# Kernel tuning notes

Measured on AMD Instinct MI355X. Metric: run time of the kernel, lower is better.

Reference implementation:

```python
import jax, jax.numpy as jnp
import numpy as np

LN_EPS = 1e-5
NORM_EPS = 1e-12


def channel_layernorm(x, w, b):
    # LayerNorm over channel dim of NCHW tensor (torch permutes to NHWC; equivalent)
    mu = x.mean(axis=1, keepdims=True)
    var = x.var(axis=1, keepdims=True)
    xn = (x - mu) / jnp.sqrt(var + LN_EPS)
    return xn * w[None, :, None, None] + b[None, :, None, None]


def pconv(x, w):
    # 1x1 pointwise conv, w: (out_ch, in_ch)
    return jnp.einsum('bchw,oc->bohw', x, w)


def dwconv3(x, w):
    # depthwise 3x3, padding 1; w: (ch, 1, 3, 3)
    return jax.lax.conv_general_dilated(
        x, w, window_strides=(1, 1), padding='SAME',
        feature_group_count=x.shape[1],
        dimension_numbers=('NCHW', 'OIHW', 'NCHW'))


def l2norm(x):
    n = jnp.sqrt(jnp.sum(x * x, axis=-1, keepdims=True))
    return x / jnp.maximum(n, NORM_EPS)


def setup_inputs() -> dict:
    key = jax.random.key(0)
    ks = jax.random.split(key, 8)
    B, C, H, W = 4, 128, 128, 128
    NH, G = 8, 2

    def w(k, shape, fan_in):
        return jax.random.normal(k, shape, dtype=jnp.float32) * (fan_in ** -0.5)

    return {
        'x': jax.random.normal(ks[0], (B, C, H, W), dtype=jnp.float32),
        'ln1_w': jnp.ones((C,), jnp.float32),
        'ln1_b': jnp.zeros((C,), jnp.float32),
        'temperature': jnp.ones((NH, 1, 1), jnp.float32),
        'qkv_p_w': w(ks[1], (3 * C, C), C),
        'qkv_d_w': w(ks[2], (3 * C, 1, 3, 3), 9),
        'proj_w': w(ks[3], (C, C), C),
        'ln2_w': jnp.ones((C,), jnp.float32),
        'ln2_b': jnp.zeros((C,), jnp.float32),
        'g1_w': w(ks[4], (2 * G * C, C), C),
        'gd_w': w(ks[5], (2 * G * C, 1, 3, 3), 9),
        'g2_w': w(ks[6], (C, G * C), G * C),
        'num_heads': NH,
    }


def reference(x, ln1_w, ln1_b, temperature, qkv_p_w, qkv_d_w, proj_w,
              ln2_w, ln2_b, g1_w, gd_w, g2_w, num_heads):
    b, c, h, w_ = x.shape
    d = c // num_heads

    # --- MDTA branch ---
    y = channel_layernorm(x, ln1_w, ln1_b)
    qkv = dwconv3(pconv(y, qkv_p_w), qkv_d_w)  # (b, 3c, h, w)
    q, k, v = jnp.split(qkv, 3, axis=1)
    q = l2norm(q.reshape(b, num_heads, d, h * w_))
    k = l2norm(k.reshape(b, num_heads, d, h * w_))
    v = v.reshape(b, num_heads, d, h * w_)
    # transposed (channel) attention: (b, heads, d, d)
    attn = jnp.einsum('bhdn,bhen->bhde', q, k) * temperature[None]
    attn = jax.nn.softmax(attn, axis=-1)
    out = jnp.einsum('bhde,bhen->bhdn', attn, v).reshape(b, c, h, w_)
    x = x + pconv(out, proj_w)

    # --- GDFN branch ---
    y = channel_layernorm(x, ln2_w, ln2_b)
    hdn = dwconv3(pconv(y, g1_w), gd_w)  # (b, 2*gamma*c, h, w)
    x1, x2 = jnp.split(hdn, 2, axis=1)
    g = jax.nn.gelu(x1, approximate=False) * x2
    x = x + pconv(g, g2_w)
    return x
```

## Files before the change

kernel.cpp:

```cpp
#include <hip/hip_runtime.h>
#include <cstdint>
#include <cstddef>

typedef float f32x4 __attribute__((ext_vector_type(4)));
typedef __bf16 bf16x8 __attribute__((ext_vector_type(8)));

__device__ __forceinline__ float b2f(unsigned short u) {
    union { unsigned int i; float f; } z; z.i = ((unsigned int)u) << 16; return z.f;
}
__device__ __forceinline__ unsigned short f2b(float f) {
    union { float f; unsigned int i; } z; z.f = f;
    unsigned int x = z.i;
    return (unsigned short)((x + 0x7FFFu + ((x >> 16) & 1u)) >> 16);
}

static constexpr int C = 128;
static constexpr int NP = 16384;
static constexpr int NH = 8;

struct Ptr11 { const float* p[11]; };
__constant__ int kWN[11]   = {128, 128, 8, 49152, 3456, 16384, 128, 128, 65536, 4608, 32768};
__constant__ int kWOff[11] = {0, 128, 256, 272, 49424, 52880, 69264, 69392, 69520, 135056, 139664};
static constexpr int kWTotal = 172432;

__global__ __launch_bounds__(256)
void cvt_w_kernel(Ptr11 P, unsigned short* __restrict__ dst)
{
    int seg = blockIdx.y;
    int n = kWN[seg];
    int i = blockIdx.x * 256 + threadIdx.x;
    if (i >= n) return;
    dst[kWOff[seg] + i] = f2b(P.p[seg][i]);
}

__device__ __forceinline__ void dw8(const unsigned short* base, int y, int xi,
                                    const float* wr, float* o)
{
    uint4 rv0 = uint4{0,0,0,0}, rv1, rv2 = uint4{0,0,0,0};
    if (y > 0)   rv0 = *(const uint4*)(base - 128);
    rv1 = *(const uint4*)(base);
    if (y < 127) rv2 = *(const uint4*)(base + 128);
    uint4 rows[3] = {rv0, rv1, rv2};
    #pragma unroll
    for (int j = 0; j < 8; ++j) o[j] = 0.f;
    #pragma unroll
    for (int r = 0; r < 3; ++r) {
        union { uint4 v; unsigned short u[8]; } cv; cv.v = rows[r];
        int lh = __shfl_up((int)cv.u[7], 1, 16);
        int rh = __shfl_down((int)cv.u[0], 1, 16);
        float p[10];
        p[0] = (xi > 0)   ? b2f((unsigned short)lh) : 0.f;
        p[9] = (xi < 120) ? b2f((unsigned short)rh) : 0.f;
        #pragma unroll
        for (int j = 0; j < 8; ++j) p[j + 1] = b2f(cv.u[j]);
        #pragma unroll
        for (int j = 0; j < 8; ++j)
            o[j] += wr[r * 3] * p[j] + wr[r * 3 + 1] * p[j + 1] + wr[r * 3 + 2] * p[j + 2];
    }
}

template <int COUT>
__device__ __forceinline__ void gemm_core_tr(
    const unsigned short* BsT,
    const unsigned short* __restrict__ W,
    unsigned short* __restrict__ OutB,
    int n0, int tid)
{
    const int lane = tid & 63;
    const int wid  = tid >> 6;
    const int ln16 = lane & 15, quad = lane >> 4;
    const int wy = wid >> 1, wx = wid & 1;
    const char* bs = (const char*)BsT;
    const int swz = (ln16 & 7) << 4;
    int rbase[4];
    #pragma unroll
    for (int nt = 0; nt < 4; ++nt) {
        int n = wx * 64 + nt * 16 + ln16;
        rbase[nt] = n * 256 + quad * 16;
    }

    for (int cc = 0; cc < COUT / 128; ++cc) {
        const int m0 = cc * 128;
        f32x4 acc[4][4];
        #pragma unroll
        for (int i = 0; i < 4; ++i)
            #pragma unroll
            for (int j = 0; j < 4; ++j) acc[i][j] = f32x4{0.f, 0.f, 0.f, 0.f};

        #pragma unroll
        for (int k0 = 0; k0 < 128; k0 += 32) {
            bf16x8 afr[4], bfr[4];
            #pragma unroll
            for (int mt = 0; mt < 4; ++mt) {
                int m = m0 + wy * 64 + mt * 16 + ln16;
                uint4 v = *(const uint4*)(W + (size_t)m * 128 + k0 + quad * 8);
                afr[mt] = *(bf16x8*)&v;
            }
            #pragma unroll
            for (int nt = 0; nt < 4; ++nt) {
                uint4 v = *(const uint4*)(bs + ((rbase[nt] + k0 * 2) ^ swz));
                bfr[nt] = *(bf16x8*)&v;
            }
            #pragma unroll
            for (int mt = 0; mt < 4; ++mt)
                #pragma unroll
                for (int nt = 0; nt < 4; ++nt)
                    acc[mt][nt] = __builtin_amdgcn_mfma_f32_16x16x32_bf16(
                        afr[mt], bfr[nt], acc[mt][nt], 0, 0, 0);
        }
        #pragma unroll
        for (int mt = 0; mt < 4; ++mt)
            #pragma unroll
            for (int nt = 0; nt < 4; ++nt) {
                int co0 = m0 + wy * 64 + mt * 16 + quad * 4;
                int n = n0 + wx * 64 + nt * 16 + ln16;
                #pragma unroll
                for (int r = 0; r < 4; ++r)
                    OutB[(size_t)(co0 + r) * NP + n] = f2b(acc[mt][nt][r]);
            }
    }
}

template <int COUT>
__global__ __launch_bounds__(256)
void lngemm_kernel(const float* __restrict__ x,
                   const unsigned short* __restrict__ lg,
                   const unsigned short* __restrict__ lb,
                   const unsigned short* __restrict__ W,
                   unsigned short* __restrict__ Out)
{
    __shared__ unsigned short BsT[128 * 128];
    __shared__ float Ssum[8][128], Ssq[8][128], Mu[128], Rs[128];
    const int tid = threadIdx.x;
    const int b = blockIdx.y;
    const int n0 = blockIdx.x * 128;
    const int pxg = tid & 31;
    const int cseg = tid >> 5;
    const float* xb = x + (size_t)b * C * NP + n0 + pxg * 4;

    f32x4 hv[16];
    f32x4 vs = f32x4{0.f, 0.f, 0.f, 0.f}, vq = f32x4{0.f, 0.f, 0.f, 0.f};
    #pragma unroll
    for (int i = 0; i < 16; ++i) {
        f32x4 v = *(const f32x4*)(xb + (size_t)(cseg * 16 + i) * NP);
        hv[i] = v; vs += v; vq += v * v;
    }
    #pragma unroll
    for (int j = 0; j < 4; ++j) {
        Ssum[cseg][pxg * 4 + j] = vs[j];
        Ssq[cseg][pxg * 4 + j]  = vq[j];
    }
    __syncthreads();
    if (tid < 128) {
        float s = 0.f, q = 0.f;
        #pragma unroll
        for (int e = 0; e < 8; ++e) { s += Ssum[e][tid]; q += Ssq[e][tid]; }
        float mu = s * (1.f / 128.f);
        float var = q * (1.f / 128.f) - mu * mu;
        Mu[tid] = mu;
        Rs[tid] = rsqrtf(fmaxf(var, 0.f) + 1e-5f);
    }
    __syncthreads();
    f32x4 mu4 = *(const f32x4*)(&Mu[pxg * 4]);
    f32x4 rs4 = *(const f32x4*)(&Rs[pxg * 4]);

    float gwv[16], bwv[16];
    #pragma unroll
    for (int i = 0; i < 16; ++i) {
        gwv[i] = b2f(lg[cseg * 16 + i]);
        bwv[i] = b2f(lb[cseg * 16 + i]);
    }

    char* p = (char*)BsT;
    #pragma unroll
    for (int j = 0; j < 4; ++j) {
        int n = pxg * 4 + j;
        union { uint4 v[2]; unsigned short u[16]; } o;
        #pragma unroll
        for (int i = 0; i < 16; ++i)
            o.u[i] = f2b((hv[i][j] - mu4[j]) * rs4[j] * gwv[i] + bwv[i]);
        int base = n * 256 + cseg * 32;
        int sw = (n & 7) << 4;
        *(uint4*)(p + (base ^ sw))        = o.v[0];
        *(uint4*)(p + ((base + 16) ^ sw)) = o.v[1];
    }
    __syncthreads();
    gemm_core_tr<COUT>(BsT, W, Out + (size_t)b * COUT * NP, n0, tid);
}

template <int COUT>
__global__ __launch_bounds__(256)
void gemm_bf16t_kernel(const unsigned short* __restrict__ W,
                       const unsigned short* __restrict__ Xt,
                       unsigned short* __restrict__ Out)
{
    __shared__ unsigned short BsT[128 * 128];
    const int tid = threadIdx.x;
    const int b = blockIdx.y;
    const int n0 = blockIdx.x * 128;
    const unsigned short* Xb = Xt + (size_t)b * NP * 128 + (size_t)n0 * 128;
    char* p = (char*)BsT;
    #pragma unroll
    for (int r = 0; r < 8; ++r) {
        int flat = tid + r * 256;
        int n = flat >> 4, ks = flat & 15;
        uint4 v = *(const uint4*)(Xb + (size_t)n * 128 + ks * 8);
        *(uint4*)(p + ((n * 256 + ks * 16) ^ ((n & 7) << 4))) = v;
    }
    __syncthreads();
    gemm_core_tr<COUT>(BsT, W, Out + (size_t)b * COUT * NP, n0, tid);
}

__global__ __launch_bounds__(256)
void dwqkgram_kernel(const unsigned short* __restrict__ big,
                     const unsigned short* __restrict__ w9,
                     float* __restrict__ Spart,
                     float* __restrict__ Npart)
{
    __shared__ unsigned short qs_[16 * 520];
    __shared__ unsigned short ks_[16 * 520];
    __shared__ float Sred[4][256];
    const int h = blockIdx.x, b = blockIdx.y, sp = blockIdx.z;
    const int tid = threadIdx.x;
    const int wid = tid >> 6, lane = tid & 63;
    const int xi = (tid & 15) * 8;
    const int yr = (tid >> 4) & 3;
    const int y  = sp * 4 + yr;
    const int bh = b * NH + h;
    float* Np = Npart + ((size_t)bh * 32 + sp) * 32;

    #pragma unroll
    for (int p = 0; p < 4; ++p) {
        int qc = p * 4 + wid;
        #pragma unroll
        for (int s = 0; s < 2; ++s) {
            int ch = s * 128 + h * 16 + qc;
            const unsigned short* base = big + ((size_t)b * 384 + ch) * NP + y * 128 + xi;
            float wr[9];
            #pragma unroll
            for (int i = 0; i < 9; ++i) wr[i] = b2f(w9[ch * 9 + i]);
            float o[8];
            dw8(base, y, xi, wr, o);
            union { uint4 v; unsigned short u[8]; } res;
            float ss = 0.f;
            #pragma unroll
            for (int j = 0; j < 8; ++j) {
                res.u[j] = f2b(o[j]);
                float vv = b2f(res.u[j]);
                ss += vv * vv;
            }
            unsigned short* tile = s ? ks_ : qs_;
            *(uint4*)(&tile[qc * 520 + yr * 128 + xi]) = res.v;
            #pragma unroll
            for (int od = 32; od > 0; od >>= 1) ss += __shfl_xor(ss, od, 64);
            if (lane == 0) Np[s * 16 + qc] = ss;
        }
    }
    __syncthreads();

    const int ln16 = lane & 15, quad = lane >> 4;
    f32x4 acc = f32x4{0.f, 0.f, 0.f, 0.f};
    #pragma unroll
    for (int i = 0; i < 4; ++i) {
        int off = wid * 128 + i * 32 + quad * 8;
        uint4 qv = *(const uint4*)(&qs_[ln16 * 520 + off]);
        uint4 kv = *(const uint4*)(&ks_[ln16 * 520 + off]);
        acc = __builtin_amdgcn_mfma_f32_16x16x32_bf16(*(bf16x8*)&qv, *(bf16x8*)&kv, acc, 0, 0, 0);
    }
    #pragma unroll
    for (int r = 0; r < 4; ++r) Sred[wid][(quad * 4 + r) * 16 + ln16] = acc[r];
    __syncthreads();
    float ssum = Sred[0][tid] + Sred[1][tid] + Sred[2][tid] + Sred[3][tid];
    Spart[((size_t)bh * 32 + sp) * 256 + tid] = ssum;
}

__global__ __launch_bounds__(256)
void softwp_kernel(const float* __restrict__ Spart, const float* __restrict__ Npart,
                   const unsigned short* __restrict__ temp,
                   const unsigned short* __restrict__ proj,
                   unsigned short* __restrict__ W2)
{
    __shared__ float Ps[256];
    int bh = blockIdx.x;
    int b = bh >> 3, h = bh & 7;
    int t = threadIdx.x;
    int dq = t >> 4, dk = t & 15;
    float sacc = 0.f;
    const float* Sp = Spart + (size_t)bh * 32 * 256;
    #pragma unroll
    for (int j = 0; j < 32; ++j) sacc += Sp[j * 256 + t];
    const float* Np = Npart + (size_t)bh * 32 * 32;
    float sq = 0.f, sk = 0.f;
    #pragma unroll
    for (int sp = 0; sp < 32; ++sp) { sq += Np[sp * 32 + dq]; sk += Np[sp * 32 + 16 + dk]; }
    float nq = fmaxf(sqrtf(sq), 1e-12f);
    float nk = fmaxf(sqrtf(sk), 1e-12f);
    float v = sacc / (nq * nk) * b2f(temp[h]);
    float m = v;
    #pragma unroll
    for (int o = 8; o > 0; o >>= 1) m = fmaxf(m, __shfl_xor(m, o, 16));
    float e = __expf(v - m);
    float s = e;
    #pragma unroll
    for (int o = 8; o > 0; o >>= 1) s += __shfl_xor(s, o, 16);
    Ps[t] = e / s;
    __syncthreads();

    int co = t >> 1;
    int eo = (t & 1) * 8;
    union { uint4 v[2]; unsigned short u[16]; } pw;
    pw.v[0] = *(const uint4*)(proj + (size_t)co * 128 + h * 16);
    pw.v[1] = *(const uint4*)(proj + (size_t)co * 128 + h * 16 + 8);
    float prw[16];
    #pragma unroll
    for (int d = 0; d < 16; ++d) prw[d] = b2f(pw.u[d]);
    union { uint4 v; unsigned short u[8]; } o8;
    #pragma unroll
    for (int j = 0; j < 8; ++j) {
        int ee = eo + j;
        float s2 = 0.f;
        #pragma unroll
        for (int d = 0; d < 16; ++d) s2 += prw[d] * Ps[d * 16 + ee];
        o8.u[j] = f2b(s2);
    }
    *(uint4*)(W2 + ((size_t)b * 128 + co) * 128 + h * 16 + eo) = o8.v;
}

__global__ __launch_bounds__(256)
void projln_kernel(const unsigned short* __restrict__ W2,
                   const unsigned short* __restrict__ big,
                   const unsigned short* __restrict__ w9,
                   const float* __restrict__ Res,
                   unsigned short* __restrict__ Xmid,
                   const unsigned short* __restrict__ lg,
                   const unsigned short* __restrict__ lb,
                   unsigned short* __restrict__ Y2t)
{
    __shared__ unsigned short Bs[128][130];
    __shared__ float RedS[2][128], RedQ[2][128], Mu[128], Rs[128];
    const int tid = threadIdx.x;
    const int b = blockIdx.y;
    const int y = blockIdx.x;
    const int n0 = y * 128;
    const unsigned short* Wb = W2 + (size_t)b * 16384;

    {
        const int xi = (tid & 15) * 8;
        const int crow = tid >> 4;
        #pragma unroll
        for (int p = 0; p < 8; ++p) {
            int c = p * 16 + crow;
            int ch = 256 + c;
            const unsigned short* base = big + ((size_t)b * 384 + ch) * NP + n0 + xi;
            float wr[9];
            #pragma unroll
            for (int i = 0; i < 9; ++i) wr[i] = b2f(w9[ch * 9 + i]);
            float o[8];
            dw8(base, y, xi, wr, o);
            union { uint4 v; unsigned int d[4]; unsigned short u[8]; } res;
            #pragma unroll
            for (int j = 0; j < 8; ++j) res.u[j] = f2b(o[j]);
            unsigned int* d = (unsigned int*)&Bs[c][xi];
            d[0] = res.d[0]; d[1] = res.d[1]; d[2] = res.d[2]; d[3] = res.d[3];
        }
    }
    __syncthreads();

    const int lane = tid & 63, wid = tid >> 6;
    const int ln16 = lane & 15, quad = lane >> 4;
    const int wy = wid >> 1, wx = wid & 1;

    f32x4 acc[4][4];
    #pragma unroll
    for (int i = 0; i < 4; ++i)
        #pragma unroll
        for (int j = 0; j < 4; ++j) acc[i][j] = f32x4{0.f, 0.f, 0.f, 0.f};

    #pragma unroll
    for (int k0 = 0; k0 < 128; k0 += 32) {
        bf16x8 afr[4], bfr[4];
        #pragma unroll
        for (int mt = 0; mt < 4; ++mt) {
            int m = wy * 64 + mt * 16 + ln16;
            uint4 v = *(const uint4*)(Wb + (size_t)m * 128 + k0 + quad * 8);
            afr[mt] = *(bf16x8*)&v;
        }
        #pragma unroll
        for (int nt = 0; nt < 4; ++nt) {
            int n = wx * 64 + nt * 16 + ln16;
            union { bf16x8 v; unsigned short u[8]; } tmp;
            #pragma unroll
            for (int j = 0; j < 8; ++j) tmp.u[j] = Bs[k0 + quad * 8 + j][n];
            bfr[nt] = tmp.v;
        }
        #pragma unroll
        for (int mt = 0; mt < 4; ++mt)
            #pragma unroll
            for (int nt = 0; nt < 4; ++nt)
                acc[mt][nt] = __builtin_amdgcn_mfma_f32_16x16x32_bf16(
                    afr[mt], bfr[nt], acc[mt][nt], 0, 0, 0);
    }

    size_t base = (size_t)b * 128 * NP;
    float ps[4] = {0.f, 0.f, 0.f, 0.f}, pq[4] = {0.f, 0.f, 0.f, 0.f};
    #pragma unroll
    for (int mt = 0; mt < 4; ++mt)
        #pragma unroll
        for (int nt = 0; nt < 4; ++nt) {
            int co0 = wy * 64 + mt * 16 + quad * 4;
            int n = n0 + wx * 64 + nt * 16 + ln16;
            #pragma unroll
            for (int r = 0; r < 4; ++r) {
                size_t idx = base + (size_t)(co0 + r) * NP + n;
                float tv = Res[idx] + acc[mt][nt][r];
                Xmid[idx] = f2b(tv);
                acc[mt][nt][r] = tv;
                ps[nt] += tv; pq[nt] += tv * tv;
            }
        }
    #pragma unroll
    for (int nt = 0; nt < 4; ++nt) {
        ps[nt] += __shfl_xor(ps[nt], 16, 64); ps[nt] += __shfl_xor(ps[nt], 32, 64);
        pq[nt] += __shfl_xor(pq[nt], 16, 64); pq[nt] += __shfl_xor(pq[nt], 32, 64);
    }
    if (quad == 0) {
        #pragma unroll
        for (int nt = 0; nt < 4; ++nt) {
            int nn = wx * 64 + nt * 16 + ln16;
            RedS[wy][nn] = ps[nt]; RedQ[wy][nn] = pq[nt];
        }
    }
    __syncthreads();
    if (tid < 128) {
        float s = RedS[0][tid] + RedS[1][tid];
        float q = RedQ[0][tid] + RedQ[1][tid];
        float mu = s * (1.f / 128.f);
        float var = q * (1.f / 128.f) - mu * mu;
        Mu[tid] = mu; Rs[tid] = rsqrtf(fmaxf(var, 0.f) + 1e-5f);
    }
    __syncthreads();

    char* p = (char*)Bs;
    #pragma unroll
    for (int mt = 0; mt < 4; ++mt) {
        int co0 = wy * 64 + mt * 16 + quad * 4;
        union { uint2 v; unsigned short u[4]; } gv, bv;
        gv.v = *(const uint2*)(lg + co0);
        bv.v = *(const uint2*)(lb + co0);
        float gw[4], bw[4];
        #pragma unroll
        for (int r = 0; r < 4; ++r) { gw[r] = b2f(gv.u[r]); bw[r] = b2f(bv.u[r]); }
        #pragma unroll
        for (int nt = 0; nt < 4; ++nt) {
            int nn = wx * 64 + nt * 16 + ln16;
            float mu = Mu[nn], rs = Rs[nn];
            union { uint2 v; unsigned short u[4]; } t2;
            #pragma unroll
            for (int r = 0; r < 4; ++r)
                t2.u[r] = f2b((acc[mt][nt][r] - mu) * rs * gw[r] + bw[r]);
            int addr = (nn * 256 + co0 * 2) ^ ((nn & 7) << 4);
            *(uint2*)(p + addr) = t2.v;
        }
    }
    __syncthreads();

    unsigned short* Yo = Y2t + (size_t)b * NP * 128 + (size_t)n0 * 128;
    #pragma unroll
    for (int r = 0; r < 8; ++r) {
        int flat = tid + r * 256;
        int n = flat >> 4, ks = flat & 15;
        uint4 v = *(const uint4*)(p + ((n * 256 + ks * 16) ^ ((n & 7) << 4)));
        *(uint4*)(Yo + (size_t)n * 128 + ks * 8) = v;
    }
}

template <int K>
__global__ __launch_bounds__(256)
void gemm_pconv(const unsigned short* __restrict__ W,
                const unsigned short* __restrict__ X,
                float* __restrict__ Out,
                const unsigned short* __restrict__ Res,
                int Cout)
{
    __shared__ unsigned short Bs[32][130];
    const int tid = threadIdx.x;
    const int b = blockIdx.z;
    const int n0 = blockIdx.x * 128;
    const int m0 = blockIdx.y * 128;
    const unsigned short* Xb = X + (size_t)b * K * NP;
    const int wid = tid >> 6;
    const int lane = tid & 63;
    const int ln16 = lane & 15;
    const int quad = lane >> 4;
    const int wy = wid >> 1;
    const int wx = wid & 1;

    f32x4 acc[4][4];
    #pragma unroll
    for (int i = 0; i < 4; ++i)
        #pragma unroll
        for (int j = 0; j < 4; ++j)
            acc[i][j] = f32x4{0.f, 0.f, 0.f, 0.f};

    for (int k0 = 0; k0 < K; k0 += 32) {
        #pragma unroll
        for (int r = 0; r < 2; ++r) {
            int flat = tid + r * 256;
            int kk = flat >> 4;
            int nn = (flat & 15) * 8;
            uint4 v = *(const uint4*)(Xb + (size_t)(k0 + kk) * NP + n0 + nn);
            unsigned int* d = (unsigned int*)&Bs[kk][nn];
            d[0] = v.x; d[1] = v.y; d[2] = v.z; d[3] = v.w;
        }
        __syncthreads();

        bf16x8 afr[4];
        #pragma unroll
        for (int mt = 0; mt < 4; ++mt) {
            int m = m0 + wy * 64 + mt * 16 + ln16;
            uint4 v = *(const uint4*)(W + (size_t)m * K + k0 + quad * 8);
            afr[mt] = *(bf16x8*)&v;
        }
        bf16x8 bfr[4];
        #pragma unroll
        for (int nt = 0; nt < 4; ++nt) {
            int n = wx * 64 + nt * 16 + ln16;
            union { bf16x8 v; unsigned short u[8]; } tmp;
            #pragma unroll
            for (int j = 0; j < 8; ++j) tmp.u[j] = Bs[quad * 8 + j][n];
            bfr[nt] = tmp.v;
        }
        #pragma unroll
        for (int mt = 0; mt < 4; ++mt)
            #pragma unroll
            for (int nt = 0; nt < 4; ++nt)
                acc[mt][nt] = __builtin_amdgcn_mfma_f32_16x16x32_bf16(
                    afr[mt], bfr[nt], acc[mt][nt], 0, 0, 0);
        __syncthreads();
    }

    size_t outbase = (size_t)b * Cout * NP;
    #pragma unroll
    for (int mt = 0; mt < 4; ++mt) {
        #pragma unroll
        for (int nt = 0; nt < 4; ++nt) {
            int co0 = m0 + wy * 64 + mt * 16 + quad * 4;
            int n = n0 + wx * 64 + nt * 16 + ln16;
            #pragma unroll
            for (int r = 0; r < 4; ++r) {
                size_t idx = outbase + (size_t)(co0 + r) * NP + n;
                Out[idx] = b2f(Res[idx]) + acc[mt][nt][r];
            }
        }
    }
}

__global__ __launch_bounds__(256)
void dwgelu_kernel(const unsigned short* __restrict__ hdn,
                   const unsigned short* __restrict__ w9,
                   unsigned short* __restrict__ g)
{
    int t = blockIdx.x * 256 + threadIdx.x;
    int xi = (t & 15) * 8;
    int y  = (t >> 4) & 127;
    int bc = t >> 11;
    int c  = bc & 255;
    int b  = bc >> 8;
    const unsigned short* base1 = hdn + ((size_t)b * 512 + c) * NP + y * 128 + xi;
    const unsigned short* base2 = base1 + (size_t)256 * NP;

    float w1[9], w2[9];
    #pragma unroll
    for (int i = 0; i < 9; ++i) {
        w1[i] = b2f(w9[c * 9 + i]);
        w2[i] = b2f(w9[(c + 256) * 9 + i]);
    }

    float a1[8], a2[8];
    dw8(base1, y, xi, w1, a1);
    dw8(base2, y, xi, w2, a2);

    union { uint4 v; unsigned short u[8]; } res;
    #pragma unroll
    for (int j = 0; j < 8; ++j) {
        float u = a1[j];
        float tt = u * (0.7978845608f + 0.0356774081f * u * u);
        float e = __expf(2.f * tt);
        float th = 1.f - 2.f / (e + 1.f);
        float ge = 0.5f * u * (1.f + th);
        res.u[j] = f2b(ge * a2[j]);
    }
    *(uint4*)(g + (size_t)bc * NP + y * 128 + xi) = res.v;
}

struct Bufs {
    unsigned short* xmid;
    unsigned short* y2;
    unsigned short* big;
    unsigned short* mid;
    float* Spart;
    float* Npart;
    unsigned short* W2;
};

static void run_pipeline(const float* x_f32, float* out_f32,
                         const unsigned short* w,
                         const Bufs& B, int nb, hipStream_t stream)
{
    const unsigned short* ln1_w   = w + 0;
    const unsigned short* ln1_b   = w + 128;
    const unsigned short* temp    = w + 256;
    const unsigned short* qkv_p_w = w + 272;
    const unsigned short* qkv_d_w = w + 49424;
    const unsigned short* proj_w  = w + 52880;
    const unsigned short* ln2_w   = w + 69264;
    const unsigned short* ln2_b   = w + 69392;
    const unsigned short* g1_w    = w + 69520;
    const unsigned short* gd_w    = w + 135056;
    const unsigned short* g2_w    = w + 139664;

    lngemm_kernel<384><<<dim3(NP / 128, nb), 256, 0, stream>>>(x_f32, ln1_w, ln1_b, qkv_p_w, B.big);
    dwqkgram_kernel<<<dim3(NH, nb, 32), 256, 0, stream>>>(B.big, qkv_d_w, B.Spart, B.Npart);
    softwp_kernel<<<nb * NH, 256, 0, stream>>>(B.Spart, B.Npart, temp, proj_w, B.W2);
    projln_kernel<<<dim3(NP / 128, nb), 256, 0, stream>>>(B.W2, B.big, qkv_d_w, x_f32,
                                                          B.xmid, ln2_w, ln2_b, B.y2);

    gemm_bf16t_kernel<512><<<dim3(NP / 128, nb), 256, 0, stream>>>(g1_w, B.y2, B.big);
    dwgelu_kernel<<<nb * 256 * NP / 2048, 256, 0, stream>>>(B.big, gd_w, B.mid);
    gemm_pconv<256><<<dim3(NP / 128, 1, nb), 256, 0, stream>>>(g2_w, B.mid, out_f32, B.xmid, 128);
}

extern "C" void kernel_launch(void* const* d_in, const int* in_sizes, int n_in,
                              void* d_out, int out_size, void* d_ws, size_t ws_size,
                              hipStream_t stream)
{
    (void)in_sizes; (void)n_in; (void)out_size;
    const float* x = (const float*)d_in[0];
    char* ws = (char*)d_ws;

    size_t off = 0;
    unsigned short* wpack = (unsigned short*)(ws + off);
    off += (size_t)kWTotal * 2;
    off = (off + 255) & ~(size_t)255;
    size_t header = off;

    auto layout = [&](int nb, size_t o, Bufs& B) -> size_t {
        B.xmid = (unsigned short*)(ws + o);  o += (size_t)nb * C * NP * 2;
        B.y2   = (unsigned short*)(ws + o);  o += (size_t)nb * C * NP * 2;
        B.big  = (unsigned short*)(ws + o);  o += (size_t)nb * 512 * NP * 2;
        B.mid  = (unsigned short*)(ws + o);  o += (size_t)nb * 256 * NP * 2;
        B.Spart = (float*)(ws + o);          o += (size_t)nb * NH * 32 * 256 * 4;
        B.Npart = (float*)(ws + o);          o += (size_t)nb * NH * 32 * 32 * 4;
        B.W2   = (unsigned short*)(ws + o);  o += (size_t)nb * 128 * 128 * 2;
        return o;
    };

    Ptr11 P;
    for (int i = 0; i < 11; ++i) P.p[i] = (const float*)d_in[i + 1];
    cvt_w_kernel<<<dim3(256, 11), 256, 0, stream>>>(P, wpack);

    Bufs Bfull;
    size_t need_full = layout(4, header, Bfull);

    if (ws_size >= need_full) {
        run_pipeline(x, (float*)d_out, wpack, Bfull, 4, stream);
    } else {
        Bufs B1;
        layout(1, header, B1);
        for (int b = 0; b < 4; ++b) {
            run_pipeline(x + (size_t)b * C * NP,
                         (float*)d_out + (size_t)b * C * NP,
                         wpack, B1, 1, stream);
        }
    }
}
```

Baseline: 248.6 us.

## Fold LayerNorm affine into QKV weights and apply mean/rstd in GEMM epilogue

The first LayerNorm+QKV projection no longer normalizes activations before the GEMM. The LN gain is folded into the bf16 weights, and row sums and bias projections are precomputed. Mean and rstd are applied per pixel in the epilogue, so raw x is cast to bf16 straight into shared memory. The tile shrinks to 64 pixels for more blocks, with a new swizzle and shuffle-based stat reduction. This cuts the per-element normalize math and shrinks LDS, but raw unnormalized bf16 inputs and the subtract-after-GEMM form can lose precision.

```diff
diff --git a/kernel.cpp b/kernel.cpp
--- a/kernel.cpp
+++ b/kernel.cpp
@@ -18,6 +18,8 @@
 static constexpr int NP = 16384;
 static constexpr int NH = 8;
 
+#define SWZ(n) ((((n) ^ ((n) >> 3)) & 7) << 4)
+
 struct Ptr11 { const float* p[11]; };
 __constant__ int kWN[11]   = {128, 128, 8, 49152, 3456, 16384, 128, 128, 65536, 4608, 32768};
 __constant__ int kWOff[11] = {0, 128, 256, 272, 49424, 52880, 69264, 69392, 69520, 135056, 139664};
@@ -30,7 +32,26 @@
     int n = kWN[seg];
     int i = blockIdx.x * 256 + threadIdx.x;
     if (i >= n) return;
-    dst[kWOff[seg] + i] = f2b(P.p[seg][i]);
+    float v = P.p[seg][i];
+    if (seg == 3) v *= P.p[0][i & 127];
+    dst[kWOff[seg] + i] = f2b(v);
+}
+
+__global__ __launch_bounds__(128)
+void prep_lnw_kernel(const float* __restrict__ w,
+                     const float* __restrict__ g,
+                     const float* __restrict__ bb,
+                     float* __restrict__ Saux, float* __restrict__ Kaux)
+{
+    int o = blockIdx.x * 128 + threadIdx.x;
+    if (o >= 384) return;
+    float s = 0.f, k = 0.f;
+    for (int c = 0; c < 128; ++c) {
+        float wv = w[o * 128 + c];
+        s += b2f(f2b(wv * g[c]));
+        k += wv * bb[c];
+    }
+    Saux[o] = s; Kaux[o] = k;
 }
 
 __device__ __forceinline__ void dw8(const unsigned short* base, int y, int xi,
@@ -59,6 +80,120 @@
     }
 }
 
+__global__ __launch_bounds__(256)
+void lngemm_fused(const float* __restrict__ x,
+                  const unsigned short* __restrict__ Wt,
+                  const float* __restrict__ Saux,
+                  const float* __restrict__ Kaux,
+                  unsigned short* __restrict__ Out)
+{
+    __shared__ unsigned short BsT[64 * 128];
+    __shared__ float LSum[4][64], LSq[4][64], Mu[64], Rs[64];
+    const int tid = threadIdx.x;
+    const int b = blockIdx.y;
+    const int n0 = blockIdx.x * 64;
+    const int pxg = tid & 15;
+    const int cseg = tid >> 4;
+    const int lane = tid & 63;
+    const float* xb = x + (size_t)b * C * NP + n0 + pxg * 4;
+    char* p = (char*)BsT;
+
+    f32x4 vs = f32x4{0.f,0.f,0.f,0.f}, vq = f32x4{0.f,0.f,0.f,0.f};
+    {
+        f32x4 hv[8];
+        #pragma unroll
+        for (int i = 0; i < 8; ++i) {
+            f32x4 v = *(const f32x4*)(xb + (size_t)(cseg * 8 + i) * NP);
+            hv[i] = v; vs += v; vq += v * v;
+        }
+        #pragma unroll
+        for (int j = 0; j < 4; ++j) {
+            int n = pxg * 4 + j;
+            union { uint4 v; unsigned short u[8]; } o;
+            #pragma unroll
+            for (int i = 0; i < 8; ++i) o.u[i] = f2b(hv[i][j]);
+            *(uint4*)(p + ((n * 256 + cseg * 16) ^ SWZ(n))) = o.v;
+        }
+    }
+    #pragma unroll
+    for (int j = 0; j < 4; ++j) {
+        vs[j] += __shfl_xor(vs[j], 16, 64); vq[j] += __shfl_xor(vq[j], 16, 64);
+        vs[j] += __shfl_xor(vs[j], 32, 64); vq[j] += __shfl_xor(vq[j], 32, 64);
+    }
+    if (lane < 16) {
+        int wv = tid >> 6;
+        #pragma unroll
+        for (int j = 0; j < 4; ++j) { LSum[wv][pxg * 4 + j] = vs[j]; LSq[wv][pxg * 4 + j] = vq[j]; }
+    }
+    __syncthreads();
+    if (tid < 64) {
+        float s = LSum[0][tid] + LSum[1][tid] + LSum[2][tid] + LSum[3][tid];
+        float q = LSq[0][tid] + LSq[1][tid] + LSq[2][tid] + LSq[3][tid];
+        float mu = s * (1.f / 128.f);
+        float var = q * (1.f / 128.f) - mu * mu;
+        Mu[tid] = mu; Rs[tid] = rsqrtf(fmaxf(var, 0.f) + 1e-5f);
+    }
+    __syncthreads();
+
+    const int wid = tid >> 6;
+    const int ln16 = lane & 15, quad = lane >> 4;
+    const int wy = wid >> 1, wx = wid & 1;
+    int rbase[2], swz[2];
+    #pragma unroll
+    for (int nt = 0; nt < 2; ++nt) {
+        int n = wx * 32 + nt * 16 + ln16;
+        rbase[nt] = n * 256 + quad * 16;
+        swz[nt] = SWZ(n);
+    }
+    size_t ob = (size_t)b * 384 * NP;
+    #pragma unroll
+    for (int cc = 0; cc < 3; ++cc) {
+        const unsigned short* Wc = Wt + (size_t)cc * 128 * 128;
+        f32x4 acc[4][2];
+        #pragma unroll
+        for (int i = 0; i < 4; ++i)
+            #pragma unroll
+            for (int j = 0; j < 2; ++j) acc[i][j] = f32x4{0.f, 0.f, 0.f, 0.f};
+
+        #pragma unroll
+        for (int k0 = 0; k0 < 128; k0 += 32) {
+            bf16x8 afr[4], bfr[2];
+            #pragma unroll
+            for (int mt = 0; mt < 4; ++mt) {
+                int m = wy * 64 + mt * 16 + ln16;
+                uint4 v = *(const uint4*)(Wc + (size_t)m * 128 + k0 + quad * 8);
+                afr[mt] = *(bf16x8*)&v;
+            }
+            #pragma unroll
+            for (int nt = 0; nt < 2; ++nt) {
+                uint4 v = *(const uint4*)(p + ((rbase[nt] + k0 * 2) ^ swz[nt]));
+                bfr[nt] = *(bf16x8*)&v;
+            }
+            #pragma unroll
+            for (int mt = 0; mt < 4; ++mt)
+                #pragma unroll
+                for (int nt = 0; nt < 2; ++nt)
+                    acc[mt][nt] = __builtin_amdgcn_mfma_f32_16x16x32_bf16(
+                        afr[mt], bfr[nt], acc[mt][nt], 0, 0, 0);
+        }
+        #pragma unroll
+        for (int mt = 0; mt < 4; ++mt) {
+            int co0 = cc * 128 + wy * 64 + mt * 16 + quad * 4;
+            f32x4 S4 = *(const f32x4*)(Saux + co0);
+            f32x4 K4 = *(const f32x4*)(Kaux + co0);
+            #pragma unroll
+            for (int nt = 0; nt < 2; ++nt) {
+                int nn = wx * 32 + nt * 16 + ln16;
+                float mu = Mu[nn], rs = Rs[nn];
+                #pragma unroll
+                for (int r = 0; r < 4; ++r)
+                    Out[ob + (size_t)(co0 + r) * NP + n0 + nn] =
+                        f2b(rs * (acc[mt][nt][r] - mu * S4[r]) + K4[r]);
+            }
+        }
+    }
+}
+
 template <int COUT>
 __device__ __forceinline__ void gemm_core_tr(
     const unsigned short* BsT,
@@ -119,73 +254,6 @@
                     OutB[(size_t)(co0 + r) * NP + n] = f2b(acc[mt][nt][r]);
             }
     }
-}
-
-template <int COUT>
-__global__ __launch_bounds__(256)
-void lngemm_kernel(const float* __restrict__ x,
-                   const unsigned short* __restrict__ lg,
-                   const unsigned short* __restrict__ lb,
-                   const unsigned short* __restrict__ W,
-                   unsigned short* __restrict__ Out)
-{
-    __shared__ unsigned short BsT[128 * 128];
-    __shared__ float Ssum[8][128], Ssq[8][128], Mu[128], Rs[128];
-    const int tid = threadIdx.x;
-    const int b = blockIdx.y;
-    const int n0 = blockIdx.x * 128;
-    const int pxg = tid & 31;
-    const int cseg = tid >> 5;
-    const float* xb = x + (size_t)b * C * NP + n0 + pxg * 4;
-
-    f32x4 hv[16];
-    f32x4 vs = f32x4{0.f, 0.f, 0.f, 0.f}, vq = f32x4{0.f, 0.f, 0.f, 0.f};
-    #pragma unroll
-    for (int i = 0; i < 16; ++i) {
-        f32x4 v = *(const f32x4*)(xb + (size_t)(cseg * 16 + i) * NP);
-        hv[i] = v; vs += v; vq += v * v;
-    }
-    #pragma unroll
-    for (int j = 0; j < 4; ++j) {
-        Ssum[cseg][pxg * 4 + j] = vs[j];
-        Ssq[cseg][pxg * 4 + j]  = vq[j];
-    }
-    __syncthreads();
-    if (tid < 128) {
-        float s = 0.f, q = 0.f;
-        #pragma unroll
-        for (int e = 0; e < 8; ++e) { s += Ssum[e][tid]; q += Ssq[e][tid]; }
-        float mu = s * (1.f / 128.f);
-        float var = q * (1.f / 128.f) - mu * mu;
-        Mu[tid] = mu;
-        Rs[tid] = rsqrtf(fmaxf(var, 0.f) + 1e-5f);
-    }
-    __syncthreads();
-    f32x4 mu4 = *(const f32x4*)(&Mu[pxg * 4]);
-    f32x4 rs4 = *(const f32x4*)(&Rs[pxg * 4]);
-
-    float gwv[16], bwv[16];
-    #pragma unroll
-    for (int i = 0; i < 16; ++i) {
-        gwv[i] = b2f(lg[cseg * 16 + i]);
-        bwv[i] = b2f(lb[cseg * 16 + i]);
-    }
-
-    char* p = (char*)BsT;
-    #pragma unroll
-    for (int j = 0; j < 4; ++j) {
-        int n = pxg * 4 + j;
-        union { uint4 v[2]; unsigned short u[16]; } o;
-        #pragma unroll
-        for (int i = 0; i < 16; ++i)
-            o.u[i] = f2b((hv[i][j] - mu4[j]) * rs4[j] * gwv[i] + bwv[i]);
-        int base = n * 256 + cseg * 32;
-        int sw = (n & 7) << 4;
-        *(uint4*)(p + (base ^ sw))        = o.v[0];
-        *(uint4*)(p + ((base + 16) ^ sw)) = o.v[1];
-    }
-    __syncthreads();
-    gemm_core_tr<COUT>(BsT, W, Out + (size_t)b * COUT * NP, n0, tid);
 }
 
 template <int COUT>
@@ -605,10 +673,9 @@
 
 static void run_pipeline(const float* x_f32, float* out_f32,
                          const unsigned short* w,
+                         const float* Saux, const float* Kaux,
                          const Bufs& B, int nb, hipStream_t stream)
 {
-    const unsigned short* ln1_w   = w + 0;
-    const unsigned short* ln1_b   = w + 128;
     const unsigned short* temp    = w + 256;
     const unsigned short* qkv_p_w = w + 272;
     const unsigned short* qkv_d_w = w + 49424;
@@ -619,7 +686,7 @@
     const unsigned short* gd_w    = w + 135056;
     const unsigned short* g2_w    = w + 139664;
 
-    lngemm_kernel<384><<<dim3(NP / 128, nb), 256, 0, stream>>>(x_f32, ln1_w, ln1_b, qkv_p_w, B.big);
+    lngemm_fused<<<dim3(NP / 64, nb), 256, 0, stream>>>(x_f32, qkv_p_w, Saux, Kaux, B.big);
     dwqkgram_kernel<<<dim3(NH, nb, 32), 256, 0, stream>>>(B.big, qkv_d_w, B.Spart, B.Npart);
     softwp_kernel<<<nb * NH, 256, 0, stream>>>(B.Spart, B.Npart, temp, proj_w, B.W2);
     projln_kernel<<<dim3(NP / 128, nb), 256, 0, stream>>>(B.W2, B.big, qkv_d_w, x_f32,
@@ -641,6 +708,9 @@
     size_t off = 0;
     unsigned short* wpack = (unsigned short*)(ws + off);
     off += (size_t)kWTotal * 2;
+    off = (off + 255) & ~(size_t)255;
+    float* Saux = (float*)(ws + off);  off += 384 * 4;
+    float* Kaux = (float*)(ws + off);  off += 384 * 4;
     off = (off + 255) & ~(size_t)255;
     size_t header = off;
 
@@ -658,19 +728,21 @@
     Ptr11 P;
     for (int i = 0; i < 11; ++i) P.p[i] = (const float*)d_in[i + 1];
     cvt_w_kernel<<<dim3(256, 11), 256, 0, stream>>>(P, wpack);
+    prep_lnw_kernel<<<3, 128, 0, stream>>>((const float*)d_in[4], (const float*)d_in[1],
+                                           (const float*)d_in[2], Saux, Kaux);
 
     Bufs Bfull;
     size_t need_full = layout(4, header, Bfull);
 
     if (ws_size >= need_full) {
-        run_pipeline(x, (float*)d_out, wpack, Bfull, 4, stream);
+        run_pipeline(x, (float*)d_out, wpack, Saux, Kaux, Bfull, 4, stream);
     } else {
         Bufs B1;
         layout(1, header, B1);
         for (int b = 0; b < 4; ++b) {
             run_pipeline(x + (size_t)b * C * NP,
                          (float*)d_out + (size_t)b * C * NP,
-                         wpack, B1, 1, stream);
-        }
-    }
-}
+                         wpack, Saux, Kaux, B1, 1, stream);
+        }
+    }
+}
```

Result: slower. 259.2 us (+4.3%).
